# Optimization experiments

Hardware: AMD Instinct MI355X
Metric: run time of the kernel (lower is better)

## Reference

```python
import jax, jax.numpy as jnp
import numpy as np

B, DIM, RES = 32, 384, 28
KEY_DIM, HEADS, RATIO = 32, 8, 4
D = RATIO * KEY_DIM            # 128 value dim per head
DH = D * HEADS                 # 1024
NHKD = KEY_DIM * HEADS         # 256
H_QKV = DH + 2 * NHKD          # 1536
N = RES * RES                  # 784 tokens
EPS = 1e-5
SCALE = KEY_DIM ** -0.5


def _bias_idxs():
    pts = [(i, j) for i in range(RES) for j in range(RES)]
    offs, idxs = {}, []
    for p1 in pts:
        for p2 in pts:
            o = (abs(p1[0] - p2[0]), abs(p1[1] - p2[1]))
            if o not in offs:
                offs[o] = len(offs)
            idxs.append(offs[o])
    return np.asarray(idxs, np.int32).reshape(N, N), len(offs)


def hardswish(x):
    return x * jnp.clip(x + 3.0, 0.0, 6.0) * (1.0 / 6.0)


def bn_eval(x, g, b, m, v):
    # inference-mode BatchNorm2d over channel axis 1
    s = (g / jnp.sqrt(v + EPS))[None, :, None, None]
    return (x - m[None, :, None, None]) * s + b[None, :, None, None]


def setup_inputs() -> dict:
    key = jax.random.key(0)
    ks = jax.random.split(key, 12)
    idxs, n_off = _bias_idxs()
    return {
        "x": jax.random.normal(ks[0], (B, DIM, RES, RES), jnp.float32),
        "qkv_w": jax.random.normal(ks[1], (H_QKV, DIM), jnp.float32) * 0.02,
        "qkv_g": jax.random.uniform(ks[2], (H_QKV,), jnp.float32, 0.5, 1.5),
        "qkv_b": jax.random.normal(ks[3], (H_QKV,), jnp.float32) * 0.1,
        "qkv_m": jax.random.normal(ks[4], (H_QKV,), jnp.float32) * 0.1,
        "qkv_v": jax.random.uniform(ks[5], (H_QKV,), jnp.float32, 0.5, 1.5),
        "attn_biases": jax.random.normal(ks[6], (HEADS, n_off), jnp.float32) * 0.02,
        "proj_w": jax.random.normal(ks[7], (DIM, DH), jnp.float32) * 0.02,
        "proj_g": jax.random.uniform(ks[8], (DIM,), jnp.float32, 0.5, 1.5),
        "proj_b": jax.random.normal(ks[9], (DIM,), jnp.float32) * 0.1,
        "proj_m": jax.random.normal(ks[10], (DIM,), jnp.float32) * 0.1,
        "proj_v": jax.random.uniform(ks[11], (DIM,), jnp.float32, 0.5, 1.5),
        "bias_idxs": jnp.asarray(idxs),
    }


def reference(x, qkv_w, qkv_g, qkv_b, qkv_m, qkv_v, attn_biases,
              proj_w, proj_g, proj_b, proj_m, proj_v, bias_idxs):
    Bb, C, Hh, Ww = x.shape
    n = Hh * Ww
    # qkv: 1x1 conv + BN + hardswish
    y = jnp.einsum('bchw,oc->bohw', x, qkv_w)
    y = hardswish(bn_eval(y, qkv_g, qkv_b, qkv_m, qkv_v))
    y = y.reshape(Bb, HEADS, H_QKV // HEADS, n)
    q, k, v = jnp.split(y, [KEY_DIM, 2 * KEY_DIM], axis=2)  # [B,h,kd,N] x2, [B,h,d,N]
    bias = attn_biases[:, bias_idxs]                         # [heads, N, N]
    attn = jnp.einsum('bhkn,bhkm->bhnm', q, k) * SCALE + bias[None]
    attn = jax.nn.softmax(attn, axis=-1)
    out = jnp.einsum('bhdm,bhnm->bhdn', v, attn)             # v @ attn^T
    out = out.reshape(Bb, DH, Hh, Ww)
    # proj: hardswish -> 1x1 conv + BN + hardswish
    out = hardswish(out)
    out = jnp.einsum('bchw,oc->bohw', out, proj_w)
    out = hardswish(bn_eval(out, proj_g, proj_b, proj_m, proj_v))
    return out
```

## Files before the change

kernel.cpp:

```cpp
#include <hip/hip_runtime.h>
#include <cstdint>

constexpr int BATCH = 32;
constexpr int DIMC  = 384;
constexpr int NTOK  = 784;
constexpr int KD    = 32;
constexpr int DV    = 128;
constexpr int PERH  = 192;
constexpr int HQKV  = 1536;
constexpr int DHTOT = 1024;
constexpr int NMC   = 25;
constexpr int VPB   = NMC * 8 * 512;
constexpr float BNEPS  = 1e-5f;
constexpr float QSCALE = 0.17677669529663687f;
constexpr float LOG2E  = 1.4426950408889634f;

#define DEVFN static __device__ __forceinline__

using f16x8 = __attribute__((ext_vector_type(8))) _Float16;
using f32x4 = __attribute__((ext_vector_type(4))) float;

DEVFN float hswish(float x) {
  float t = fminf(fmaxf(x + 3.0f, 0.0f), 6.0f);
  return x * t * (1.0f / 6.0f);
}
DEVFN uint16_t f2h(float f) { return __builtin_bit_cast(uint16_t, (_Float16)f); }
DEVFN float h2f(uint16_t u) { return (float)__builtin_bit_cast(_Float16, u); }

DEVFN void gload16(const void* g, void* l) {
  __builtin_amdgcn_global_load_lds(
      (const __attribute__((address_space(1))) void*)g,
      (__attribute__((address_space(3))) void*)l, 16, 0, 0);
}

__global__ __launch_bounds__(256) void convert_w(
    const float* __restrict__ qw, const float* __restrict__ pw,
    uint16_t* __restrict__ qwh, uint16_t* __restrict__ pwh)
{
  constexpr int QW4 = (HQKV * DIMC) / 4;
  constexpr int PW4 = (DIMC * DHTOT) / 4;
  int idx = blockIdx.x * 256 + threadIdx.x;
  if (idx < QW4) {
    float4 v = reinterpret_cast<const float4*>(qw)[idx];
    uint2 p;
    p.x = (uint32_t)f2h(v.x) | ((uint32_t)f2h(v.y) << 16);
    p.y = (uint32_t)f2h(v.z) | ((uint32_t)f2h(v.w) << 16);
    reinterpret_cast<uint2*>(qwh)[idx] = p;
  } else if (idx < QW4 + PW4) {
    int i2 = idx - QW4;
    float4 v = reinterpret_cast<const float4*>(pw)[i2];
    uint2 p;
    p.x = (uint32_t)f2h(v.x) | ((uint32_t)f2h(v.y) << 16);
    p.y = (uint32_t)f2h(v.z) | ((uint32_t)f2h(v.w) << 16);
    reinterpret_cast<uint2*>(pwh)[i2] = p;
  }
}

__global__ __launch_bounds__(256) void bias_build(
    const float* __restrict__ biases, uint16_t* __restrict__ biasH)
{
  const int n = blockIdx.x, h = blockIdx.y;
  const int t = threadIdx.x;
  if (t >= 196) return;
  const int m0 = 4*t;
  const int ri = (n * 2341) >> 16;
  const int rj = n - ri*28;
  const float* bh_ = biases + (size_t)h * NTOK;
  uint16_t o[4];
  #pragma unroll
  for (int r = 0; r < 4; ++r) {
    int m  = m0 + r;
    int im = (m * 2341) >> 16;
    int jm = m - im*28;
    int di = ri - im; di = di < 0 ? -di : di;
    int dj = rj - jm; dj = dj < 0 ? -dj : dj;
    o[r] = f2h(bh_[di*28 + dj]);
  }
  uint2 p;
  p.x = (uint32_t)o[0] | ((uint32_t)o[1] << 16);
  p.y = (uint32_t)o[2] | ((uint32_t)o[3] << 16);
  *reinterpret_cast<uint2*>(biasH + ((size_t)h*NTOK + n)*NTOK + m0) = p;
}

__global__ __launch_bounds__(256) void transpose_x(
    const float* __restrict__ x, uint16_t* __restrict__ xT)
{
  const int b = blockIdx.z, n0 = blockIdx.x * 32, c0 = blockIdx.y * 32;
  __shared__ float t[32][33];
  const int tx = threadIdx.x & 31, ty = threadIdx.x >> 5;
  const float* xb = x + (size_t)b * DIMC * NTOK;
  #pragma unroll
  for (int k = 0; k < 4; ++k) {
    int c = c0 + ty + 8*k;
    int n = n0 + tx;
    t[ty + 8*k][tx] = (n < NTOK) ? xb[(size_t)c * NTOK + n] : 0.f;
  }
  __syncthreads();
  uint16_t* xTb = xT + (size_t)b * NTOK * DIMC;
  #pragma unroll
  for (int k = 0; k < 4; ++k) {
    int n = n0 + ty + 8*k;
    if (n < NTOK) xTb[(size_t)n * DIMC + c0 + tx] = f2h(t[tx][ty + 8*k]);
  }
}

__global__ __launch_bounds__(256) void qkv_gemm(
    const uint16_t* __restrict__ wh, const uint16_t* __restrict__ xT,
    const float* __restrict__ gw, const float* __restrict__ bw,
    const float* __restrict__ mw, const float* __restrict__ vw,
    uint16_t* __restrict__ qb, uint16_t* __restrict__ kb, uint16_t* __restrict__ vb)
{
  const int b  = blockIdx.z;
  const int m0 = blockIdx.y * 128;
  const int n0 = blockIdx.x * 64;
  __shared__ __align__(16) uint16_t As[2][128*64];
  __shared__ __align__(16) uint16_t Bs[2][64*64];

  const int tid = threadIdx.x;
  const int w = tid >> 6, l = tid & 63, lg = l >> 4, ln = l & 15;
  const int wr = w >> 1, wc = w & 1;
  const int wbase = tid & 192;
  const uint16_t* xb = xT + (size_t)b * NTOK * DIMC;

  f32x4 acc[4][2];
  #pragma unroll
  for (int mi = 0; mi < 4; ++mi)
    #pragma unroll
    for (int ni = 0; ni < 2; ++ni) acc[mi][ni] = (f32x4){0.f,0.f,0.f,0.f};

  auto stage = [&](int buf, int k0) {
    #pragma unroll
    for (int j = 0; j < 4; ++j) {
      int s = j*256 + tid;
      int row = s >> 3, sl = s & 7;
      int srck = k0 + 8 * (sl ^ (row & 7));
      gload16(wh + (size_t)(m0 + row) * DIMC + srck,
              &As[buf][(j*256 + wbase) * 8]);
    }
    #pragma unroll
    for (int j = 0; j < 2; ++j) {
      int s = j*256 + tid;
      int row = s >> 3, sl = s & 7;
      int nrow = n0 + row; if (nrow > NTOK-1) nrow = NTOK-1;
      int srck = k0 + 8 * (sl ^ (row & 7));
      gload16(xb + (size_t)nrow * DIMC + srck,
              &Bs[buf][(j*256 + wbase) * 8]);
    }
  };

  stage(0, 0);
  int cur = 0;
  for (int k0 = 0; k0 < DIMC; k0 += 64) {
    __syncthreads();
    if (k0 + 64 < DIMC) stage(cur ^ 1, k0 + 64);
    #pragma unroll
    for (int kk = 0; kk < 2; ++kk) {
      f16x8 af[4], bf[2];
      #pragma unroll
      for (int mi = 0; mi < 4; ++mi) {
        int row = 64*wr + 16*mi + ln;
        int slot = (4*kk + lg) ^ (row & 7);
        af[mi] = *reinterpret_cast<const f16x8*>(&As[cur][row*64 + slot*8]);
      }
      #pragma unroll
      for (int ni = 0; ni < 2; ++ni) {
        int row = 32*wc + 16*ni + ln;
        int slot = (4*kk + lg) ^ (row & 7);
        bf[ni] = *reinterpret_cast<const f16x8*>(&Bs[cur][row*64 + slot*8]);
      }
      #pragma unroll
      for (int mi = 0; mi < 4; ++mi)
        #pragma unroll
        for (int ni = 0; ni < 2; ++ni)
          acc[mi][ni] = __builtin_amdgcn_mfma_f32_16x16x32_f16(
              af[mi], bf[ni], acc[mi][ni], 0, 0, 0);
    }
    cur ^= 1;
  }

  #pragma unroll
  for (int mi = 0; mi < 4; ++mi) {
    const int ob = m0 + 64*wr + 16*mi;
    const int h  = ob / PERH;
    const int r0 = ob - h * PERH;
    const int bh = b*8 + h;
    float sc[4], sh[4];
    #pragma unroll
    for (int r = 0; r < 4; ++r) {
      int o = ob + 4*lg + r;
      float s = gw[o] * rsqrtf(vw[o] + BNEPS);
      sc[r] = s; sh[r] = bw[o] - mw[o]*s;
    }
    #pragma unroll
    for (int ni = 0; ni < 2; ++ni) {
      int n = n0 + 32*wc + 16*ni + ln;
      if (n >= NTOK) continue;
      float v4[4];
      #pragma unroll
      for (int r = 0; r < 4; ++r) v4[r] = hswish(acc[mi][ni][r]*sc[r] + sh[r]);
      if (r0 < 2*KD) {
        if (r0 < KD) {
          #pragma unroll
          for (int r = 0; r < 4; ++r) v4[r] *= QSCALE;
        }
        uint16_t* base = (r0 < KD) ? qb : kb;
        int dd = (r0 & 16) + 4*lg;
        uint2 p;
        p.x = (uint32_t)f2h(v4[0]) | ((uint32_t)f2h(v4[1]) << 16);
        p.y = (uint32_t)f2h(v4[2]) | ((uint32_t)f2h(v4[3]) << 16);
        *reinterpret_cast<uint2*>(base + ((size_t)bh*NTOK + n)*KD + dd) = p;
      } else {
        const int dv0 = r0 - 2*KD;
        const int mc = n >> 5, mm = n & 31;
        const int lgv = mm >> 3, jj = mm & 7;
        uint16_t* vblk = vb + (size_t)bh*VPB + ((size_t)mc*8)*512 + lgv*128 + jj;
        #pragma unroll
        for (int r = 0; r < 4; ++r) {
          int dv = dv0 + 4*lg + r;
          int dt = dv >> 4, lnv = dv & 15;
          vblk[(size_t)dt*512 + lnv*8] = f2h(v4[r]);
        }
      }
    }
  }
}

__global__ __launch_bounds__(256) void attn_kernel(
    const uint16_t* __restrict__ Qb, const uint16_t* __restrict__ Kb,
    const uint16_t* __restrict__ Vb, const uint16_t* __restrict__ biasH,
    uint16_t* __restrict__ a2T)
{
  const int bh = blockIdx.y;
  const int b_ = bh >> 3;
  const int h  = bh & 7;

  __shared__ __align__(16) uint16_t plds[4][2][16][72];

  const int tid = threadIdx.x;
  const int w   = tid >> 6;
  const int l   = tid & 63;
  const int lg  = l >> 4;
  const int ln  = l & 15;

  const int tile = blockIdx.x * 4 + w;
  if (tile >= 25) return;
  const int n0 = tile * 32;
  const int nA = n0 + ln;
  int nBr = n0 + 16 + ln;
  const int nB = (nBr < NTOK) ? nBr : (NTOK-1);

  const uint16_t* Kbase = Kb + (size_t)bh * NTOK * KD;
  const uint16_t* Vbase = Vb + (size_t)bh * VPB;
  const uint16_t* browA = biasH + ((size_t)h * NTOK + nA) * NTOK;
  const uint16_t* browB = biasH + ((size_t)h * NTOK + nB) * NTOK;

  const f16x8 qfA = *reinterpret_cast<const f16x8*>(
      Qb + ((size_t)bh*NTOK + nA)*KD + 8*lg);
  const f16x8 qfB = *reinterpret_cast<const f16x8*>(
      Qb + ((size_t)bh*NTOK + nB)*KD + 8*lg);

  float MA = -1e30f, LA = 0.f, MB = -1e30f, LB = 0.f;
  f32x4 accA[8], accB[8];
  #pragma unroll
  for (int dt = 0; dt < 8; ++dt) {
    accA[dt] = (f32x4){0.f,0.f,0.f,0.f};
    accB[dt] = (f32x4){0.f,0.f,0.f,0.f};
  }

  for (int mb = 0; mb < NTOK; mb += 64) {
    const int rem   = (NTOK - mb) >> 4;
    const int ntile = rem < 4 ? rem : 4;
    const int mc0   = mb >> 5;

    float pA[16], pB[16];
    #pragma unroll
    for (int i = 0; i < 16; ++i) { pA[i] = -1e30f; pB[i] = -1e30f; }

    #pragma unroll
    for (int t = 0; t < 4; ++t) {
      if (t < ntile) {
        f16x8 kf = *reinterpret_cast<const f16x8*>(
            Kbase + (size_t)(mb + 16*t + ln)*KD + 8*lg);
        uint2 ba = *reinterpret_cast<const uint2*>(browA + mb + 16*t + 4*lg);
        uint2 bb = *reinterpret_cast<const uint2*>(browB + mb + 16*t + 4*lg);
        f32x4 cA, cB;
        cA[0] = h2f((uint16_t)(ba.x & 0xffffu)); cA[1] = h2f((uint16_t)(ba.x >> 16));
        cA[2] = h2f((uint16_t)(ba.y & 0xffffu)); cA[3] = h2f((uint16_t)(ba.y >> 16));
        cB[0] = h2f((uint16_t)(bb.x & 0xffffu)); cB[1] = h2f((uint16_t)(bb.x >> 16));
        cB[2] = h2f((uint16_t)(bb.y & 0xffffu)); cB[3] = h2f((uint16_t)(bb.y >> 16));
        f32x4 sA = __builtin_amdgcn_mfma_f32_16x16x32_f16(kf, qfA, cA, 0, 0, 0);
        f32x4 sB = __builtin_amdgcn_mfma_f32_16x16x32_f16(kf, qfB, cB, 0, 0, 0);
        #pragma unroll
        for (int r = 0; r < 4; ++r) { pA[4*t+r] = sA[r]; pB[4*t+r] = sB[r]; }
      }
    }

    f16x8 vf0[8];
    #pragma unroll
    for (int dt = 0; dt < 8; ++dt)
      vf0[dt] = *reinterpret_cast<const f16x8*>(
          Vbase + ((size_t)mc0*8 + dt)*512 + l*8);

    float mxA = pA[0], mxB = pB[0];
    #pragma unroll
    for (int i = 1; i < 16; ++i) { mxA = fmaxf(mxA, pA[i]); mxB = fmaxf(mxB, pB[i]); }
    mxA = fmaxf(mxA, __shfl_xor(mxA, 16)); mxA = fmaxf(mxA, __shfl_xor(mxA, 32));
    mxB = fmaxf(mxB, __shfl_xor(mxB, 16)); mxB = fmaxf(mxB, __shfl_xor(mxB, 32));

    float MnA = fmaxf(MA, mxA), MnB = fmaxf(MB, mxB);
    float alA = exp2f((MA - MnA) * LOG2E), alB = exp2f((MB - MnB) * LOG2E);
    float sumA = 0.f, sumB = 0.f;
    #pragma unroll
    for (int i = 0; i < 16; ++i) {
      pA[i] = exp2f((pA[i] - MnA) * LOG2E); sumA += pA[i];
      pB[i] = exp2f((pB[i] - MnB) * LOG2E); sumB += pB[i];
    }
    sumA += __shfl_xor(sumA, 16); sumA += __shfl_xor(sumA, 32);
    sumB += __shfl_xor(sumB, 16); sumB += __shfl_xor(sumB, 32);
    LA = LA * alA + sumA; MA = MnA;
    LB = LB * alB + sumB; MB = MnB;

    float alA4[4], alB4[4];
    #pragma unroll
    for (int r = 0; r < 4; ++r) {
      alA4[r] = __shfl(alA, 20*lg + r);
      alB4[r] = __shfl(alB, 20*lg + r);
    }
    #pragma unroll
    for (int dt = 0; dt < 8; ++dt) {
      #pragma unroll
      for (int r = 0; r < 4; ++r) { accA[dt][r] *= alA4[r]; accB[dt][r] *= alB4[r]; }
    }

    #pragma unroll
    for (int t = 0; t < 4; ++t) {
      uint2 ka, kb2;
      ka.x  = (uint32_t)f2h(pA[4*t+0]) | ((uint32_t)f2h(pA[4*t+1]) << 16);
      ka.y  = (uint32_t)f2h(pA[4*t+2]) | ((uint32_t)f2h(pA[4*t+3]) << 16);
      kb2.x = (uint32_t)f2h(pB[4*t+0]) | ((uint32_t)f2h(pB[4*t+1]) << 16);
      kb2.y = (uint32_t)f2h(pB[4*t+2]) | ((uint32_t)f2h(pB[4*t+3]) << 16);
      *reinterpret_cast<uint2*>(&plds[w][0][ln][16*t + 4*lg]) = ka;
      *reinterpret_cast<uint2*>(&plds[w][1][ln][16*t + 4*lg]) = kb2;
    }

    {
      f16x8 pfA = *reinterpret_cast<const f16x8*>(&plds[w][0][ln][8*lg]);
      f16x8 pfB = *reinterpret_cast<const f16x8*>(&plds[w][1][ln][8*lg]);
      __builtin_amdgcn_s_setprio(1);
      #pragma unroll
      for (int dt = 0; dt < 8; ++dt) {
        accA[dt] = __builtin_amdgcn_mfma_f32_16x16x32_f16(pfA, vf0[dt], accA[dt], 0, 0, 0);
        accB[dt] = __builtin_amdgcn_mfma_f32_16x16x32_f16(pfB, vf0[dt], accB[dt], 0, 0, 0);
      }
      __builtin_amdgcn_s_setprio(0);
    }

    if (mb + 32 < NTOK) {
      f16x8 pfA = *reinterpret_cast<const f16x8*>(&plds[w][0][ln][32 + 8*lg]);
      f16x8 pfB = *reinterpret_cast<const f16x8*>(&plds[w][1][ln][32 + 8*lg]);
      f16x8 vf1[8];
      #pragma unroll
      for (int dt = 0; dt < 8; ++dt)
        vf1[dt] = *reinterpret_cast<const f16x8*>(
            Vbase + ((size_t)(mc0+1)*8 + dt)*512 + l*8);
      __builtin_amdgcn_s_setprio(1);
      #pragma unroll
      for (int dt = 0; dt < 8; ++dt) {
        accA[dt] = __builtin_amdgcn_mfma_f32_16x16x32_f16(pfA, vf1[dt], accA[dt], 0, 0, 0);
        accB[dt] = __builtin_amdgcn_mfma_f32_16x16x32_f16(pfB, vf1[dt], accB[dt], 0, 0, 0);
      }
      __builtin_amdgcn_s_setprio(0);
    }
  }

  float liA = 1.0f / LA, liB = 1.0f / LB;
  float liA4[4], liB4[4];
  #pragma unroll
  for (int r = 0; r < 4; ++r) {
    liA4[r] = __shfl(liA, 20*lg + r);
    liB4[r] = __shfl(liB, 20*lg + r);
  }
  #pragma unroll
  for (int r = 0; r < 4; ++r) {
    int rowA = n0 + 4*lg + r;
    #pragma unroll
    for (int dt = 0; dt < 8; ++dt)
      a2T[((size_t)b_*NTOK + rowA)*DHTOT + h*DV + 16*dt + ln] =
          f2h(hswish(accA[dt][r] * liA4[r]));
    int rowB = n0 + 16 + 4*lg + r;
    if (rowB < NTOK) {
      #pragma unroll
      for (int dt = 0; dt < 8; ++dt)
        a2T[((size_t)b_*NTOK + rowB)*DHTOT + h*DV + 16*dt + ln] =
            f2h(hswish(accB[dt][r] * liB4[r]));
    }
  }
}

__global__ __launch_bounds__(256) void proj_gemm(
    const uint16_t* __restrict__ wh, const uint16_t* __restrict__ a2T,
    const float* __restrict__ gw, const float* __restrict__ bw,
    const float* __restrict__ mw, const float* __restrict__ vw,
    float* __restrict__ out)
{
  const int b  = blockIdx.z;
  const int m0 = blockIdx.y * 128;
  const int n0 = blockIdx.x * 64;
  __shared__ __align__(16) uint16_t As[2][128*64];
  __shared__ __align__(16) uint16_t Bs[2][64*64];

  const int tid = threadIdx.x;
  const int w = tid >> 6, l = tid & 63, lg = l >> 4, ln = l & 15;
  const int wr = w >> 1, wc = w & 1;
  const int wbase = tid & 192;
  const uint16_t* ab = a2T + (size_t)b * NTOK * DHTOT;

  f32x4 acc[4][2];
  #pragma unroll
  for (int mi = 0; mi < 4; ++mi)
    #pragma unroll
    for (int ni = 0; ni < 2; ++ni) acc[mi][ni] = (f32x4){0.f,0.f,0.f,0.f};

  auto stage = [&](int buf, int k0) {
    #pragma unroll
    for (int j = 0; j < 4; ++j) {
      int s = j*256 + tid;
      int row = s >> 3, sl = s & 7;
      int srck = k0 + 8 * (sl ^ (row & 7));
      gload16(wh + (size_t)(m0 + row) * DHTOT + srck,
              &As[buf][(j*256 + wbase) * 8]);
    }
    #pragma unroll
    for (int j = 0; j < 2; ++j) {
      int s = j*256 + tid;
      int row = s >> 3, sl = s & 7;
      int nrow = n0 + row; if (nrow > NTOK-1) nrow = NTOK-1;
      int srck = k0 + 8 * (sl ^ (row & 7));
      gload16(ab + (size_t)nrow * DHTOT + srck,
              &Bs[buf][(j*256 + wbase) * 8]);
    }
  };

  stage(0, 0);
  int cur = 0;
  for (int k0 = 0; k0 < DHTOT; k0 += 64) {
    __syncthreads();
    if (k0 + 64 < DHTOT) stage(cur ^ 1, k0 + 64);
    #pragma unroll
    for (int kk = 0; kk < 2; ++kk) {
      f16x8 af[4], bf[2];
      #pragma unroll
      for (int mi = 0; mi < 4; ++mi) {
        int row = 64*wr + 16*mi + ln;
        int slot = (4*kk + lg) ^ (row & 7);
        af[mi] = *reinterpret_cast<const f16x8*>(&As[cur][row*64 + slot*8]);
      }
      #pragma unroll
      for (int ni = 0; ni < 2; ++ni) {
        int row = 32*wc + 16*ni + ln;
        int slot = (4*kk + lg) ^ (row & 7);
        bf[ni] = *reinterpret_cast<const f16x8*>(&Bs[cur][row*64 + slot*8]);
      }
      #pragma unroll
      for (int mi = 0; mi < 4; ++mi)
        #pragma unroll
        for (int ni = 0; ni < 2; ++ni)
          acc[mi][ni] = __builtin_amdgcn_mfma_f32_16x16x32_f16(
              af[mi], bf[ni], acc[mi][ni], 0, 0, 0);
    }
    cur ^= 1;
  }

  #pragma unroll
  for (int mi = 0; mi < 4; ++mi) {
    float sc[4], sh[4];
    #pragma unroll
    for (int r = 0; r < 4; ++r) {
      int o = m0 + 64*wr + 16*mi + 4*lg + r;
      float s = gw[o] * rsqrtf(vw[o] + BNEPS);
      sc[r] = s; sh[r] = bw[o] - mw[o]*s;
    }
    #pragma unroll
    for (int ni = 0; ni < 2; ++ni) {
      int n = n0 + 32*wc + 16*ni + ln;
      if (n >= NTOK) continue;
      #pragma unroll
      for (int r = 0; r < 4; ++r) {
        int o = m0 + 64*wr + 16*mi + 4*lg + r;
        out[((size_t)b*DIMC + o)*NTOK + n] = hswish(acc[mi][ni][r]*sc[r] + sh[r]);
      }
    }
  }
}

extern "C" void kernel_launch(void* const* d_in, const int* in_sizes, int n_in,
                              void* d_out, int out_size, void* d_ws, size_t ws_size,
                              hipStream_t stream)
{
  const float* x  = (const float*)d_in[0];
  const float* qw = (const float*)d_in[1];
  const float* qg = (const float*)d_in[2];
  const float* qb_ = (const float*)d_in[3];
  const float* qm = (const float*)d_in[4];
  const float* qv = (const float*)d_in[5];
  const float* ab = (const float*)d_in[6];
  const float* pw = (const float*)d_in[7];
  const float* pg = (const float*)d_in[8];
  const float* pb = (const float*)d_in[9];
  const float* pm = (const float*)d_in[10];
  const float* pv = (const float*)d_in[11];
  float* out = (float*)d_out;

  uint16_t* qwh   = (uint16_t*)d_ws;
  uint16_t* pwh   = qwh + (size_t)HQKV * DIMC;
  uint16_t* biasH = pwh + (size_t)DIMC * DHTOT;
  uint16_t* dyn   = biasH + (size_t)8 * NTOK * NTOK;
  const size_t fixed_bytes =
      ((size_t)HQKV*DIMC + (size_t)DIMC*DHTOT + (size_t)8*NTOK*NTOK) * 2;

  const size_t XT_B = (size_t)NTOK * DIMC;
  const size_t QK_B = (size_t)8 * NTOK * KD;
  const size_t V_B  = (size_t)8 * VPB;
  const size_t A2_B = (size_t)NTOK * DHTOT;
  const size_t PER_B = XT_B + 2*QK_B + V_B + A2_B;

  size_t avail = (ws_size > fixed_bytes) ? (ws_size - fixed_bytes) : 0;
  int nb = (int)(avail / (PER_B * 2));
  if (nb > BATCH) nb = BATCH;
  if (nb < 1) nb = 1;

  uint16_t* xTb  = dyn;
  uint16_t* qbuf = xTb  + (size_t)nb * XT_B;
  uint16_t* kbuf = qbuf + (size_t)nb * QK_B;
  uint16_t* vbuf = kbuf + (size_t)nb * QK_B;
  uint16_t* a2   = vbuf + (size_t)nb * V_B;

  convert_w<<<960, 256, 0, stream>>>(qw, pw, qwh, pwh);
  bias_build<<<dim3(NTOK, 8), 256, 0, stream>>>(ab, biasH);

  for (int b0 = 0; b0 < BATCH; b0 += nb) {
    int cb = BATCH - b0; if (cb > nb) cb = nb;
    const float* xb = x + (size_t)b0 * DIMC * NTOK;
    float* ob = out + (size_t)b0 * DIMC * NTOK;

    transpose_x<<<dim3(25, 12, cb), 256, 0, stream>>>(xb, xTb);
    qkv_gemm<<<dim3(13, 12, cb), 256, 0, stream>>>(qwh, xTb, qg, qb_, qm, qv,
                                                   qbuf, kbuf, vbuf);
    attn_kernel<<<dim3(7, cb * 8), 256, 0, stream>>>(qbuf, kbuf, vbuf, biasH, a2);
    proj_gemm<<<dim3(13, 3, cb), 256, 0, stream>>>(pwh, a2, pg, pb, pm, pv, ob);
  }
}
```

Before: 322.0 us.

## Skip online-softmax rescale when max grows little, use packed f16 convert

Adds a lazy-rescale path to the attention online softmax. When every lane's new block max is within 4 of the running max, it keeps the old max and skips the alpha exp, the shuffles and the accumulator rescaling. It also replaces the manual f32-to-f16 pack with the cvt_pkrtz intrinsic, which rounds toward zero rather than to nearest, and swaps the attention grid axes so consecutive blocks walk heads and batches instead of tiles. The lazy path lets exponentials reach up to e^4 and the conversion rounding changes slightly, both of which affect numerics.

```diff
diff --git a/kernel.cpp b/kernel.cpp
--- a/kernel.cpp
+++ b/kernel.cpp
@@ -26,6 +26,9 @@
 }
 DEVFN uint16_t f2h(float f) { return __builtin_bit_cast(uint16_t, (_Float16)f); }
 DEVFN float h2f(uint16_t u) { return (float)__builtin_bit_cast(_Float16, u); }
+DEVFN uint32_t pk2h(float a, float b) {
+  return __builtin_bit_cast(uint32_t, __builtin_amdgcn_cvt_pkrtz(a, b));
+}
 
 DEVFN void gload16(const void* g, void* l) {
   __builtin_amdgcn_global_load_lds(
@@ -43,15 +46,15 @@
   if (idx < QW4) {
     float4 v = reinterpret_cast<const float4*>(qw)[idx];
     uint2 p;
-    p.x = (uint32_t)f2h(v.x) | ((uint32_t)f2h(v.y) << 16);
-    p.y = (uint32_t)f2h(v.z) | ((uint32_t)f2h(v.w) << 16);
+    p.x = pk2h(v.x, v.y);
+    p.y = pk2h(v.z, v.w);
     reinterpret_cast<uint2*>(qwh)[idx] = p;
   } else if (idx < QW4 + PW4) {
     int i2 = idx - QW4;
     float4 v = reinterpret_cast<const float4*>(pw)[i2];
     uint2 p;
-    p.x = (uint32_t)f2h(v.x) | ((uint32_t)f2h(v.y) << 16);
-    p.y = (uint32_t)f2h(v.z) | ((uint32_t)f2h(v.w) << 16);
+    p.x = pk2h(v.x, v.y);
+    p.y = pk2h(v.z, v.w);
     reinterpret_cast<uint2*>(pwh)[i2] = p;
   }
 }
@@ -206,8 +209,8 @@
         uint16_t* base = (r0 < KD) ? qb : kb;
         int dd = (r0 & 16) + 4*lg;
         uint2 p;
-        p.x = (uint32_t)f2h(v4[0]) | ((uint32_t)f2h(v4[1]) << 16);
-        p.y = (uint32_t)f2h(v4[2]) | ((uint32_t)f2h(v4[3]) << 16);
+        p.x = pk2h(v4[0], v4[1]);
+        p.y = pk2h(v4[2], v4[3]);
         *reinterpret_cast<uint2*>(base + ((size_t)bh*NTOK + n)*KD + dd) = p;
       } else {
         const int dv0 = r0 - 2*KD;
@@ -230,7 +233,7 @@
     const uint16_t* __restrict__ Vb, const uint16_t* __restrict__ biasH,
     uint16_t* __restrict__ a2T)
 {
-  const int bh = blockIdx.y;
+  const int bh = blockIdx.x;
   const int b_ = bh >> 3;
   const int h  = bh & 7;
 
@@ -242,7 +245,7 @@
   const int lg  = l >> 4;
   const int ln  = l & 15;
 
-  const int tile = blockIdx.x * 4 + w;
+  const int tile = blockIdx.y * 4 + w;
   if (tile >= 25) return;
   const int n0 = tile * 32;
   const int nA = n0 + ln;
@@ -307,38 +310,49 @@
     mxA = fmaxf(mxA, __shfl_xor(mxA, 16)); mxA = fmaxf(mxA, __shfl_xor(mxA, 32));
     mxB = fmaxf(mxB, __shfl_xor(mxB, 16)); mxB = fmaxf(mxB, __shfl_xor(mxB, 32));
 
-    float MnA = fmaxf(MA, mxA), MnB = fmaxf(MB, mxB);
-    float alA = exp2f((MA - MnA) * LOG2E), alB = exp2f((MB - MnB) * LOG2E);
+    const bool skip = __all((mxA - MA <= 4.0f) & (mxB - MB <= 4.0f));
     float sumA = 0.f, sumB = 0.f;
-    #pragma unroll
-    for (int i = 0; i < 16; ++i) {
-      pA[i] = exp2f((pA[i] - MnA) * LOG2E); sumA += pA[i];
-      pB[i] = exp2f((pB[i] - MnB) * LOG2E); sumB += pB[i];
-    }
-    sumA += __shfl_xor(sumA, 16); sumA += __shfl_xor(sumA, 32);
-    sumB += __shfl_xor(sumB, 16); sumB += __shfl_xor(sumB, 32);
-    LA = LA * alA + sumA; MA = MnA;
-    LB = LB * alB + sumB; MB = MnB;
-
-    float alA4[4], alB4[4];
-    #pragma unroll
-    for (int r = 0; r < 4; ++r) {
-      alA4[r] = __shfl(alA, 20*lg + r);
-      alB4[r] = __shfl(alB, 20*lg + r);
-    }
-    #pragma unroll
-    for (int dt = 0; dt < 8; ++dt) {
-      #pragma unroll
-      for (int r = 0; r < 4; ++r) { accA[dt][r] *= alA4[r]; accB[dt][r] *= alB4[r]; }
+    if (skip) {
+      #pragma unroll
+      for (int i = 0; i < 16; ++i) {
+        pA[i] = exp2f((pA[i] - MA) * LOG2E); sumA += pA[i];
+        pB[i] = exp2f((pB[i] - MB) * LOG2E); sumB += pB[i];
+      }
+      sumA += __shfl_xor(sumA, 16); sumA += __shfl_xor(sumA, 32);
+      sumB += __shfl_xor(sumB, 16); sumB += __shfl_xor(sumB, 32);
+      LA += sumA; LB += sumB;
+    } else {
+      float MnA = fmaxf(MA, mxA), MnB = fmaxf(MB, mxB);
+      float alA = exp2f((MA - MnA) * LOG2E), alB = exp2f((MB - MnB) * LOG2E);
+      #pragma unroll
+      for (int i = 0; i < 16; ++i) {
+        pA[i] = exp2f((pA[i] - MnA) * LOG2E); sumA += pA[i];
+        pB[i] = exp2f((pB[i] - MnB) * LOG2E); sumB += pB[i];
+      }
+      sumA += __shfl_xor(sumA, 16); sumA += __shfl_xor(sumA, 32);
+      sumB += __shfl_xor(sumB, 16); sumB += __shfl_xor(sumB, 32);
+      LA = LA * alA + sumA; MA = MnA;
+      LB = LB * alB + sumB; MB = MnB;
+      float alA4[4], alB4[4];
+      #pragma unroll
+      for (int r = 0; r < 4; ++r) {
+        alA4[r] = __shfl(alA, 20*lg + r);
+        alB4[r] = __shfl(alB, 20*lg + r);
+      }
+      #pragma unroll
+      for (int dt = 0; dt < 8; ++dt) {
+        #pragma unroll
+        for (int r = 0; r < 4; ++r) { accA[dt][r] *= alA4[r]; accB[dt][r] *= alB4[r]; }
+      }
     }
 
     #pragma unroll
     for (int t = 0; t < 4; ++t) {
       uint2 ka, kb2;
-      ka.x  = (uint32_t)f2h(pA[4*t+0]) | ((uint32_t)f2h(pA[4*t+1]) << 16);
-      ka.y  = (uint32_t)f2h(pA[4*t+2]) | ((uint32_t)f2h(pA[4*t+3]) << 16);
-      kb2.x = (uint32_t)f2h(pB[4*t+0]) | ((uint32_t)f2h(pB[4*t+1]) << 16);
-      kb2.y = (uint32_t)f2h(pB[4*t+2]) | ((uint32_t)f2h(pB[4*t+3]) << 16);
+      ka.x  = pk2h(pA[4*t+0], pA[4*t+1]);
+      ka.y  = pk2h(pA[4*t+2], pA[4*t+3]);
+      kb2.x = pk2h(pB[4*t+0], pB[4*t+1]);
+      kb2.y = pk2h(pB[4*t+2], pB[4*t+3]);
       *reinterpret_cast<uint2*>(&plds[w][0][ln][16*t + 4*lg]) = ka;
       *reinterpret_cast<uint2*>(&plds[w][1][ln][16*t + 4*lg]) = kb2;
     }
@@ -546,7 +560,7 @@
     transpose_x<<<dim3(25, 12, cb), 256, 0, stream>>>(xb, xTb);
     qkv_gemm<<<dim3(13, 12, cb), 256, 0, stream>>>(qwh, xTb, qg, qb_, qm, qv,
                                                    qbuf, kbuf, vbuf);
-    attn_kernel<<<dim3(7, cb * 8), 256, 0, stream>>>(qbuf, kbuf, vbuf, biasH, a2);
+    attn_kernel<<<dim3(cb * 8, 7), 256, 0, stream>>>(qbuf, kbuf, vbuf, biasH, a2);
     proj_gemm<<<dim3(13, 3, cb), 256, 0, stream>>>(pwh, a2, pg, pb, pm, pv, ob);
   }
 }
```

After: 426.5 us. 32.4% more time.
